# Kernel optimization log

Measured on AMD Instinct MI355X. Metric: run time of the kernel, lower is better.

## Reference

```python
import jax, jax.numpy as jnp
import numpy as np
import math

H = 8
E = 512
D_K = E // H
NEG = -1000000000.0
# last (and only surviving) row of dist_bar: one threshold per head
DIST_BAR = np.array([0.2, 0.3, 0.4, 0.5, 0.6, 0.7, 0.8, 0.9], dtype=np.float32)


def setup_inputs() -> dict:
    key = jax.random.key(0)
    ks = jax.random.split(key, 12)
    B, N = 8, 1024
    s = 1.0 / math.sqrt(E)
    inp = {
        "query": jax.random.normal(ks[0], (B, N, E), jnp.float32),
        "key": jax.random.normal(ks[1], (B, N, E), jnp.float32),
        "value": jax.random.normal(ks[2], (B, N, E), jnp.float32),
        "dist": jax.random.uniform(ks[3], (B, 1, N, N), jnp.float32),
        "mask": jnp.ones((B, N, N), jnp.int32),
        "Wq": jax.random.normal(ks[4], (E, E), jnp.float32) * s,
        "bq": jnp.zeros((E,), jnp.float32),
        "Wk": jax.random.normal(ks[5], (E, E), jnp.float32) * s,
        "bk": jnp.zeros((E,), jnp.float32),
        "Wv": jax.random.normal(ks[6], (E, E), jnp.float32) * s,
        "bv": jnp.zeros((E,), jnp.float32),
        "Wo": jax.random.normal(ks[7], (E, E), jnp.float32) * s,
        "bo": jnp.zeros((E,), jnp.float32),
    }
    return inp


def reference(query, key, value, dist, mask, Wq, bq, Wk, bk, Wv, bv, Wo, bo):
    B, N, _ = query.shape
    # project and split heads: [B, H, N, D_K]
    def heads(x, W, b):
        return (x @ W.T + b).reshape(B, N, H, D_K).transpose(0, 2, 1, 3)
    q = heads(query, Wq, bq)
    k = heads(key, Wk, bk)
    v = heads(value, Wv, bv)
    scores = jnp.einsum("bhqd,bhkd->bhqk", q, k) / math.sqrt(D_K)
    # padding mask: [B,N,N] -> [B,1,N,N]
    scores = jnp.where(mask[:, None, :, :] == 0, NEG, scores)
    # per-head distance mask: dist [B,1,N,N] < thr[h] -> [B,H,N,N]
    thr = jnp.asarray(DIST_BAR)[None, :, None, None]
    dmask = dist < thr
    # first row/col (global atom) always attend
    dmask = dmask.at[:, :, 0, :].set(True).at[:, :, :, 0].set(True)
    scores = jnp.where(dmask, scores, NEG)
    p = jax.nn.softmax(scores, axis=-1)
    out = jnp.einsum("bhqk,bhkd->bhqd", p, v)  # [B,H,N,D_K]
    out = out.transpose(0, 2, 1, 3).reshape(B, N, H * D_K)
    return out @ Wo.T + bo
```

## Files before the change

### kernel.cpp

```cpp
#include <hip/hip_runtime.h>
#include <stdint.h>


typedef __attribute__((ext_vector_type(8))) short short8;
typedef __attribute__((ext_vector_type(4))) float floatx4;

#define MFMA16(a, b, c) __builtin_amdgcn_mfma_f32_16x16x32_bf16((a), (b), (c), 0, 0, 0)

static __device__ __forceinline__ unsigned short f2bf(float f) {
  union { float f; unsigned u; } v; v.f = f;
  unsigned r = v.u + 0x7fffu + ((v.u >> 16) & 1u);
  return (unsigned short)(r >> 16);
}

static __device__ __forceinline__ void gload_lds16(const void* g, void* l) {
  __builtin_amdgcn_global_load_lds((const __attribute__((address_space(1))) unsigned int*)g,
                                   (__attribute__((address_space(3))) unsigned int*)l,
                                   16, 0, 0);
}
static __device__ __forceinline__ int xsw(int row) { return (row & 3) ^ ((row >> 2) & 3); }

__global__ void wcast_kernel(const float* __restrict__ Wq, const float* __restrict__ Wk,
                             const float* __restrict__ Wv, const float* __restrict__ Wo,
                             unsigned short* __restrict__ o0, unsigned short* __restrict__ o1,
                             unsigned short* __restrict__ o2, unsigned short* __restrict__ o3) {
  int i = blockIdx.x * blockDim.x + threadIdx.x;
  int w = i >> 16, loc = i & 65535;
  const float* s = (w == 0) ? Wq : (w == 1) ? Wk : (w == 2) ? Wv : Wo;
  unsigned short* d = (w == 0) ? o0 : (w == 1) ? o1 : (w == 2) ? o2 : o3;
  float4 v = ((const float4*)s)[loc];
  ushort4 o;
  o.x = f2bf(v.x); o.y = f2bf(v.y); o.z = f2bf(v.z); o.w = f2bf(v.w);
  ((ushort4*)d)[loc] = o;
}

__global__ void codes_kernel(const float* __restrict__ dist, const int* __restrict__ mask,
                             unsigned char* __restrict__ codesP) {
  int t = blockIdx.x * blockDim.x + threadIdx.x;
  int flat = t << 2;
  int b = flat >> 20;
  int rem = flat & ((1 << 20) - 1);
  int row = rem >> 10;
  int col0 = rem & 1023;
  float4 d4 = ((const float4*)dist)[t];
  int4 m4 = ((const int4*)mask)[t];
  float dv[4] = {d4.x, d4.y, d4.z, d4.w};
  int mv[4] = {m4.x, m4.y, m4.z, m4.w};
  int rg = row >> 5;
  int st = (row >> 4) & 1;
  int qq = (row >> 2) & 3;
  int r = row & 3;
  size_t rowbase = (size_t)(b * 32 + rg) * 32768;
  int sub = st * 32 + r;
#pragma unroll
  for (int u = 0; u < 4; u++) {
    int col = col0 + u;
    float d = dv[u];
    int hmin = (d >= 0.2f) + (d >= 0.3f) + (d >= 0.4f) + (d >= 0.5f) +
               (d >= 0.6f) + (d >= 0.7f) + (d >= 0.8f) + (d >= 0.9f);
    unsigned char cc = (unsigned char)hmin;
    if (row == 0 || col == 0) cc = 0;
    if (mv[u] == 0) cc = 9;
    int kt = col >> 7, ci = (col >> 4) & 7, c = col & 15;
    int lane = qq * 16 + c;
    codesP[rowbase + (size_t)kt * 4096 + lane * 64 + sub + ci * 4] = cc;
  }
}

__global__ __launch_bounds__(256) void qkv_gemm(
    const float* __restrict__ Aq, const float* __restrict__ Ak, const float* __restrict__ Av,
    const unsigned short* __restrict__ Wqp, const unsigned short* __restrict__ Wkp,
    const unsigned short* __restrict__ Wvp,
    const float* __restrict__ bq, const float* __restrict__ bk, const float* __restrict__ bv,
    unsigned short* __restrict__ Qh, unsigned short* __restrict__ Kh,
    unsigned short* __restrict__ Vt) {
  const int z = blockIdx.z;
  const float* A = (z == 0) ? Aq : (z == 1) ? Ak : Av;
  const unsigned short* W = (z == 0) ? Wqp : (z == 1) ? Wkp : Wvp;
  const float* bias = (z == 0) ? bq : (z == 1) ? bk : bv;
  unsigned short* O = (z == 0) ? Qh : (z == 1) ? Kh : Vt;

  __shared__ __align__(16) short As[64 * 40];
  __shared__ __align__(16) short Bs[128 * 32];
  const int tid = threadIdx.x;
  const int lane = tid & 63;
  const int wave = tid >> 6;
  const int c = lane & 15;
  const int q = lane >> 4;
  const int m0 = blockIdx.x * 64;
  const int n0 = blockIdx.y * 128;
  const int wr = (wave >> 1) * 32;
  const int wc = (wave & 1) * 64;

  floatx4 acc[2][4];
#pragma unroll
  for (int i = 0; i < 2; i++)
#pragma unroll
    for (int j = 0; j < 4; j++) acc[i][j] = (floatx4)(0.0f);

  const int arow = tid >> 2, ach = tid & 3;
  const float* Ab = A + (size_t)(m0 + arow) * 512 + ach * 8;

  for (int k0 = 0; k0 < 512; k0 += 32) {
    __syncthreads();
#pragma unroll
    for (int it = 0; it < 2; it++) {
      int slot = wave * 128 + it * 64 + lane;
      int brow = slot >> 2, bch = slot & 3;
      int g = bch ^ xsw(brow);
      gload_lds16(W + (size_t)(n0 + brow) * 512 + k0 + g * 8,
                  &Bs[(size_t)(wave * 128 + it * 64) * 8]);
    }
    float4 a0 = *(const float4*)(Ab + k0);
    float4 a1 = *(const float4*)(Ab + k0 + 4);
    short8 av;
    av[0] = (short)f2bf(a0.x); av[1] = (short)f2bf(a0.y);
    av[2] = (short)f2bf(a0.z); av[3] = (short)f2bf(a0.w);
    av[4] = (short)f2bf(a1.x); av[5] = (short)f2bf(a1.y);
    av[6] = (short)f2bf(a1.z); av[7] = (short)f2bf(a1.w);
    *(short8*)(&As[arow * 40 + ach * 8]) = av;
    __syncthreads();

    short8 af[2], bfv[4];
#pragma unroll
    for (int i = 0; i < 2; i++)
      af[i] = *(const short8*)(&As[(wr + i * 16 + c) * 40 + q * 8]);
#pragma unroll
    for (int j = 0; j < 4; j++) {
      int row = wc + j * 16 + c;
      bfv[j] = *(const short8*)(&Bs[row * 32 + (q ^ xsw(row)) * 8]);
    }
#pragma unroll
    for (int i = 0; i < 2; i++)
#pragma unroll
      for (int j = 0; j < 4; j++)
        acc[i][j] = MFMA16(af[i], bfv[j], acc[i][j]);
  }

#pragma unroll
  for (int i = 0; i < 2; i++) {
    int gm0 = m0 + wr + i * 16 + q * 4;
#pragma unroll
    for (int j = 0; j < 4; j++) {
      int gn = n0 + wc + j * 16 + c;
      float bb = bias[gn];
      int h = gn >> 6, d = gn & 63;
      if (z == 2) {
        int b = gm0 >> 10, n = gm0 & 1023;
        ushort4 pk;
#pragma unroll
        for (int r = 0; r < 4; r++) pk[r] = f2bf(acc[i][j][r] + bb);
        *(ushort4*)(&Vt[(((size_t)(b * 8 + h) * 64 + d) << 10) + n]) = pk;
      } else {
#pragma unroll
        for (int r = 0; r < 4; r++) {
          int m = gm0 + r;
          int b = m >> 10, n = m & 1023;
          O[((((size_t)(b * 8 + h)) << 10) + n) * 64 + d] = f2bf(acc[i][j][r] + bb);
        }
      }
    }
  }
}

__global__ __launch_bounds__(256) void out_gemm(const unsigned short* __restrict__ A,
                                                const unsigned short* __restrict__ W,
                                                const float* __restrict__ bias,
                                                float* __restrict__ Out) {
  __shared__ __align__(16) short As[64 * 32];
  __shared__ __align__(16) short Bs[128 * 32];
  const int tid = threadIdx.x;
  const int lane = tid & 63;
  const int wave = tid >> 6;
  const int c = lane & 15;
  const int q = lane >> 4;
  const int m0 = blockIdx.x * 64;
  const int n0 = blockIdx.y * 128;
  const int wr = (wave >> 1) * 32;
  const int wc = (wave & 1) * 64;

  floatx4 acc[2][4];
#pragma unroll
  for (int i = 0; i < 2; i++)
#pragma unroll
    for (int j = 0; j < 4; j++) acc[i][j] = (floatx4)(0.0f);

  for (int k0 = 0; k0 < 512; k0 += 32) {
    __syncthreads();
    {
      int slot = wave * 64 + lane;
      int arow = slot >> 2, ach = slot & 3;
      int g = ach ^ xsw(arow);
      gload_lds16(A + (size_t)(m0 + arow) * 512 + k0 + g * 8, &As[(size_t)(wave * 64) * 8]);
    }
#pragma unroll
    for (int it = 0; it < 2; it++) {
      int slot = wave * 128 + it * 64 + lane;
      int brow = slot >> 2, bch = slot & 3;
      int g = bch ^ xsw(brow);
      gload_lds16(W + (size_t)(n0 + brow) * 512 + k0 + g * 8,
                  &Bs[(size_t)(wave * 128 + it * 64) * 8]);
    }
    __syncthreads();

    short8 af[2], bfv[4];
#pragma unroll
    for (int i = 0; i < 2; i++) {
      int row = wr + i * 16 + c;
      af[i] = *(const short8*)(&As[row * 32 + (q ^ xsw(row)) * 8]);
    }
#pragma unroll
    for (int j = 0; j < 4; j++) {
      int row = wc + j * 16 + c;
      bfv[j] = *(const short8*)(&Bs[row * 32 + (q ^ xsw(row)) * 8]);
    }
#pragma unroll
    for (int i = 0; i < 2; i++)
#pragma unroll
      for (int j = 0; j < 4; j++)
        acc[i][j] = MFMA16(af[i], bfv[j], acc[i][j]);
  }

#pragma unroll
  for (int i = 0; i < 2; i++) {
    int gm0 = m0 + wr + i * 16 + q * 4;
#pragma unroll
    for (int j = 0; j < 4; j++) {
      int gn = n0 + wc + j * 16 + c;
      float bb = bias[gn];
#pragma unroll
      for (int r = 0; r < 4; r++)
        Out[(size_t)(gm0 + r) * 512 + gn] = acc[i][j][r] + bb;
    }
  }
}

__global__ __launch_bounds__(256) void attn_kernel(const unsigned short* __restrict__ Qh,
                                                   const unsigned short* __restrict__ Kh,
                                                   const unsigned short* __restrict__ Vt,
                                                   const unsigned char* __restrict__ codesP,
                                                   unsigned short* __restrict__ AO) {
  __shared__ __align__(16) unsigned short P[4][32 * 132];
  const int tid = threadIdx.x;
  const int lane = tid & 63;
  const int wave = tid >> 6;
  const int c = lane & 15;
  const int q = lane >> 4;
  const int bh = blockIdx.y;
  const int b = bh >> 3;
  const int h = bh & 7;
  const size_t base = (size_t)bh << 16;
  const int rbase = blockIdx.x * 128 + wave * 32;
  const int rg = rbase >> 5;
  unsigned short* Pw = &P[wave][0];

  short8 aq[2][2];
#pragma unroll
  for (int st = 0; st < 2; st++)
#pragma unroll
    for (int kk = 0; kk < 2; kk++)
      aq[st][kk] = *(const short8*)(Qh + base + (size_t)(rbase + st * 16 + c) * 64 + kk * 32 + q * 8);

  const unsigned char* cbt = codesP + (size_t)(b * 32 + rg) * 32768 + lane * 64;
  const unsigned short* Kb = Kh + base;
  const unsigned short* Vb = Vt + base;

  float rs[2][4];
#pragma unroll
  for (int st = 0; st < 2; st++)
#pragma unroll
    for (int r = 0; r < 4; r++) rs[st][r] = 0.0f;
  floatx4 o[2][4];
#pragma unroll
  for (int st = 0; st < 2; st++)
#pragma unroll
    for (int ci = 0; ci < 4; ci++) o[st][ci] = (floatx4)(0.0f);

  for (int kt = 0; kt < 8; kt++) {
    const unsigned short* Kt = Kb + (size_t)kt * 128 * 64;
    floatx4 s[2][8];
#pragma unroll
    for (int ci = 0; ci < 8; ci++) { s[0][ci] = (floatx4)(0.0f); s[1][ci] = (floatx4)(0.0f); }
#pragma unroll
    for (int ci = 0; ci < 8; ci++)
#pragma unroll
      for (int kk = 0; kk < 2; kk++) {
        short8 bk = *(const short8*)(Kt + (size_t)(ci * 16 + c) * 64 + kk * 32 + q * 8);
        s[0][ci] = MFMA16(aq[0][kk], bk, s[0][ci]);
        s[1][ci] = MFMA16(aq[1][kk], bk, s[1][ci]);
      }
    const unsigned char* cp = cbt + (size_t)kt * 4096;
    uint4 w0 = *(const uint4*)(cp);
    uint4 w1 = *(const uint4*)(cp + 16);
    uint4 w2 = *(const uint4*)(cp + 32);
    uint4 w3 = *(const uint4*)(cp + 48);
    unsigned cv[16] = {w0.x, w0.y, w0.z, w0.w, w1.x, w1.y, w1.z, w1.w,
                       w2.x, w2.y, w2.z, w2.w, w3.x, w3.y, w3.z, w3.w};
#pragma unroll
    for (int st = 0; st < 2; st++)
#pragma unroll
      for (int ci = 0; ci < 8; ci++)
#pragma unroll
        for (int r = 0; r < 4; r++) {
          int bidx = st * 32 + ci * 4 + r;
          int code = (cv[bidx >> 2] >> ((bidx & 3) * 8)) & 0xff;
          float e = (h >= code) ? exp2f(s[st][ci][r] * 0.1803368801111362f) : 0.0f;
          rs[st][r] += e;
          Pw[(st * 16 + q * 4 + r) * 132 + ci * 16 + c] = f2bf(e);
        }
#pragma unroll
    for (int ch = 0; ch < 4; ch++) {
      short8 ap0 = *(const short8*)(&Pw[(size_t)c * 132 + ch * 32 + q * 8]);
      short8 ap1 = *(const short8*)(&Pw[(size_t)(16 + c) * 132 + ch * 32 + q * 8]);
#pragma unroll
      for (int ci = 0; ci < 4; ci++) {
        short8 bv = *(const short8*)(Vb + (size_t)(ci * 16 + c) * 1024 + kt * 128 + ch * 32 + q * 8);
        o[0][ci] = MFMA16(ap0, bv, o[0][ci]);
        o[1][ci] = MFMA16(ap1, bv, o[1][ci]);
      }
    }
  }

  float inv[2][4];
#pragma unroll
  for (int st = 0; st < 2; st++)
#pragma unroll
    for (int r = 0; r < 4; r++) {
      float v = rs[st][r];
      v += __shfl_xor(v, 1); v += __shfl_xor(v, 2);
      v += __shfl_xor(v, 4); v += __shfl_xor(v, 8);
      inv[st][r] = 1.0f / v;
    }
#pragma unroll
  for (int st = 0; st < 2; st++)
#pragma unroll
    for (int r = 0; r < 4; r++) {
      int n = rbase + st * 16 + q * 4 + r;
      size_t ob = ((size_t)((b << 10) + n)) * 512 + h * 64;
#pragma unroll
      for (int ci = 0; ci < 4; ci++)
        AO[ob + ci * 16 + c] = f2bf(o[st][ci][r] * inv[st][r]);
    }
}

extern "C" void kernel_launch(void* const* d_in, const int* in_sizes, int n_in,
                              void* d_out, int out_size, void* d_ws, size_t ws_size,
                              hipStream_t stream) {
  const float* query = (const float*)d_in[0];
  const float* key_  = (const float*)d_in[1];
  const float* value = (const float*)d_in[2];
  const float* dist  = (const float*)d_in[3];
  const int*   mask  = (const int*)d_in[4];
  const float* Wq = (const float*)d_in[5];
  const float* bq = (const float*)d_in[6];
  const float* Wk = (const float*)d_in[7];
  const float* bk = (const float*)d_in[8];
  const float* Wv = (const float*)d_in[9];
  const float* bv = (const float*)d_in[10];
  const float* Wo = (const float*)d_in[11];
  const float* bo = (const float*)d_in[12];

  char* ws = (char*)d_ws;
  size_t off = 0;
  auto alloc = [&](size_t bytes) -> char* {
    char* p = ws + off;
    off += (bytes + 255) & ~(size_t)255;
    return p;
  };
  const size_t NQKV = 8192ull * 512;
  unsigned short* wq16 = (unsigned short*)alloc(512ull * 512 * 2);
  unsigned short* wk16 = (unsigned short*)alloc(512ull * 512 * 2);
  unsigned short* wv16 = (unsigned short*)alloc(512ull * 512 * 2);
  unsigned short* wo16 = (unsigned short*)alloc(512ull * 512 * 2);
  unsigned short* Qh = (unsigned short*)alloc(NQKV * 2);
  unsigned short* Kh = (unsigned short*)alloc(NQKV * 2);
  unsigned short* Vt = (unsigned short*)alloc(NQKV * 2);
  unsigned short* AO = (unsigned short*)alloc(NQKV * 2);
  unsigned char*  codesP = (unsigned char*)alloc(8ull * 1024 * 1024);

  wcast_kernel<<<1024, 256, 0, stream>>>(Wq, Wk, Wv, Wo, wq16, wk16, wv16, wo16);
  codes_kernel<<<8192, 256, 0, stream>>>(dist, mask, codesP);
  qkv_gemm<<<dim3(128, 4, 3), 256, 0, stream>>>(query, key_, value, wq16, wk16, wv16,
                                                bq, bk, bv, Qh, Kh, Vt);
  attn_kernel<<<dim3(8, 64), 256, 0, stream>>>(Qh, Kh, Vt, codesP, AO);
  out_gemm<<<dim3(128, 4), 256, 0, stream>>>(AO, wo16, bo, (float*)d_out);
}
```

Before: 292.7 us.

## Split attention key range across wave pairs and reduce partials in LDS

Each block now covers 64 query rows instead of 128, and the four waves split into two pairs that each process half of the key tiles. The second pair writes its partial output accumulators and row sums to shared memory and the first pair adds them before normalising. This doubles the grid, which gives more blocks to spread over the GPU's compute units. It also adds a launch-bounds occupancy hint and hoists the mask-code loads ahead of the QK MFMAs. The cost is two block barriers and an LDS reduction per block, plus each Q tile being loaded by twice as many waves.

```diff
diff --git a/kernel.cpp b/kernel.cpp
--- a/kernel.cpp
+++ b/kernel.cpp
@@ -235,22 +235,24 @@
   }
 }
 
-__global__ __launch_bounds__(256) void attn_kernel(const unsigned short* __restrict__ Qh,
-                                                   const unsigned short* __restrict__ Kh,
-                                                   const unsigned short* __restrict__ Vt,
-                                                   const unsigned char* __restrict__ codesP,
-                                                   unsigned short* __restrict__ AO) {
+__global__ __launch_bounds__(256, 4) void attn_kernel(const unsigned short* __restrict__ Qh,
+                                                      const unsigned short* __restrict__ Kh,
+                                                      const unsigned short* __restrict__ Vt,
+                                                      const unsigned char* __restrict__ codesP,
+                                                      unsigned short* __restrict__ AO) {
   __shared__ __align__(16) unsigned short P[4][32 * 132];
   const int tid = threadIdx.x;
   const int lane = tid & 63;
   const int wave = tid >> 6;
+  const int wsub = wave & 1;
+  const int whalf = wave >> 1;
   const int c = lane & 15;
   const int q = lane >> 4;
   const int bh = blockIdx.y;
   const int b = bh >> 3;
   const int h = bh & 7;
   const size_t base = (size_t)bh << 16;
-  const int rbase = blockIdx.x * 128 + wave * 32;
+  const int rbase = blockIdx.x * 64 + wsub * 32;
   const int rg = rbase >> 5;
   unsigned short* Pw = &P[wave][0];
 
@@ -276,7 +278,13 @@
 #pragma unroll
     for (int ci = 0; ci < 4; ci++) o[st][ci] = (floatx4)(0.0f);
 
-  for (int kt = 0; kt < 8; kt++) {
+  for (int kti = 0; kti < 4; kti++) {
+    const int kt = whalf * 4 + kti;
+    const unsigned char* cp = cbt + (size_t)kt * 4096;
+    uint4 w0 = *(const uint4*)(cp);
+    uint4 w1 = *(const uint4*)(cp + 16);
+    uint4 w2 = *(const uint4*)(cp + 32);
+    uint4 w3 = *(const uint4*)(cp + 48);
     const unsigned short* Kt = Kb + (size_t)kt * 128 * 64;
     floatx4 s[2][8];
 #pragma unroll
@@ -289,11 +297,6 @@
         s[0][ci] = MFMA16(aq[0][kk], bk, s[0][ci]);
         s[1][ci] = MFMA16(aq[1][kk], bk, s[1][ci]);
       }
-    const unsigned char* cp = cbt + (size_t)kt * 4096;
-    uint4 w0 = *(const uint4*)(cp);
-    uint4 w1 = *(const uint4*)(cp + 16);
-    uint4 w2 = *(const uint4*)(cp + 32);
-    uint4 w3 = *(const uint4*)(cp + 48);
     unsigned cv[16] = {w0.x, w0.y, w0.z, w0.w, w1.x, w1.y, w1.z, w1.w,
                        w2.x, w2.y, w2.z, w2.w, w3.x, w3.y, w3.z, w3.w};
 #pragma unroll
@@ -319,6 +322,39 @@
         o[1][ci] = MFMA16(ap1, bv, o[1][ci]);
       }
     }
+  }
+
+  float* Pf = (float*)&P[0][0];
+  __syncthreads();
+  if (whalf == 1) {
+#pragma unroll
+    for (int st = 0; st < 2; st++)
+#pragma unroll
+      for (int ci = 0; ci < 4; ci++)
+        *(floatx4*)&Pf[(((wsub * 10 + st * 4 + ci) * 64) + lane) * 4] = o[st][ci];
+#pragma unroll
+    for (int st = 0; st < 2; st++) {
+      floatx4 rr;
+#pragma unroll
+      for (int r = 0; r < 4; r++) rr[r] = rs[st][r];
+      *(floatx4*)&Pf[(((wsub * 10 + 8 + st) * 64) + lane) * 4] = rr;
+    }
+  }
+  __syncthreads();
+  if (whalf == 1) return;
+
+#pragma unroll
+  for (int st = 0; st < 2; st++)
+#pragma unroll
+    for (int ci = 0; ci < 4; ci++) {
+      floatx4 p = *(const floatx4*)&Pf[(((wsub * 10 + st * 4 + ci) * 64) + lane) * 4];
+      o[st][ci] += p;
+    }
+#pragma unroll
+  for (int st = 0; st < 2; st++) {
+    floatx4 pr = *(const floatx4*)&Pf[(((wsub * 10 + 8 + st) * 64) + lane) * 4];
+#pragma unroll
+    for (int r = 0; r < 4; r++) rs[st][r] += pr[r];
   }
 
   float inv[2][4];
@@ -382,6 +418,6 @@
   codes_kernel<<<8192, 256, 0, stream>>>(dist, mask, codesP);
   qkv_gemm<<<dim3(128, 4, 3), 256, 0, stream>>>(query, key_, value, wq16, wk16, wv16,
                                                 bq, bk, bv, Qh, Kh, Vt);
-  attn_kernel<<<dim3(8, 64), 256, 0, stream>>>(Qh, Kh, Vt, codesP, AO);
+  attn_kernel<<<dim3(16, 64), 256, 0, stream>>>(Qh, Kh, Vt, codesP, AO);
   out_gemm<<<dim3(128, 4), 256, 0, stream>>>(AO, wo16, bo, (float*)d_out);
 }
```

Measured after the change: 305.0 us. 4.2% more time.
